# Performance work log

Measured on AMD Instinct MI355X. Metric: run time of the kernel, lower is better.

The kernel has to match this reference:

```python
import jax, jax.numpy as jnp
import numpy as np

GROUPS = 32
EPS = 1e-6  # flax.linen.GroupNorm default


def group_norm(x, scale, bias):
    B, H, W, C = x.shape
    xg = x.reshape(B, H, W, GROUPS, C // GROUPS)
    mean = jnp.mean(xg, axis=(1, 2, 4), keepdims=True)
    var = jnp.var(xg, axis=(1, 2, 4), keepdims=True)
    xn = (xg - mean) * jax.lax.rsqrt(var + EPS)
    return xn.reshape(B, H, W, C) * scale + bias


def setup_inputs() -> dict:
    key = jax.random.key(0)
    ks = jax.random.split(key, 8)
    B, H, W, C = 8, 64, 64, 128
    s = C ** -0.5  # fan-in style init scale for 1x1 conv kernels
    return {
        "x": jax.random.normal(ks[0], (B, H, W, C), dtype=jnp.float32),
        "gn_scale": jnp.ones((C,), dtype=jnp.float32),
        "gn_bias": jnp.zeros((C,), dtype=jnp.float32),
        "wq": jax.random.normal(ks[1], (C, C), dtype=jnp.float32) * s,
        "bq": jnp.zeros((C,), dtype=jnp.float32),
        "wk": jax.random.normal(ks[2], (C, C), dtype=jnp.float32) * s,
        "bk": jnp.zeros((C,), dtype=jnp.float32),
        "wv": jax.random.normal(ks[3], (C, C), dtype=jnp.float32) * s,
        "bv": jnp.zeros((C,), dtype=jnp.float32),
        "wo": jax.random.normal(ks[4], (C, C), dtype=jnp.float32) * s,
        "bo": jnp.zeros((C,), dtype=jnp.float32),
    }


def reference(x, gn_scale, gn_bias, wq, bq, wk, bk, wv, bv, wo, bo):
    B, H, W, C = x.shape
    N = H * W
    h = group_norm(x, gn_scale, gn_bias)                       # [B,H,W,C]
    hf = h.reshape(B, N, C)
    q = hf @ wq + bq                                           # 1x1 conv == per-position matmul
    k = hf @ wk + bk
    v = hf @ wv + bv
    w_ = jnp.einsum('bqd,bkd->bqk', q, k) * (C ** -0.5)        # [B,N,N] full score matrix
    w_ = jax.nn.softmax(w_, axis=2)
    o = jnp.einsum('bqk,bkd->bqd', w_, v)                      # [B,N,C]
    o = o @ wo + bo
    return x + o.reshape(B, H, W, C)
```

## Files before the change

### kernel.cpp

```cpp
#include <hip/hip_runtime.h>
#include <hip/hip_bf16.h>

#define NN 4096
#define CC 128
#define SCALE 0.088388347648318447f
#define LOG2E 1.4426950408889634f

typedef __attribute__((ext_vector_type(8))) short short8v;
typedef __attribute__((ext_vector_type(4))) float f32x4;
typedef __attribute__((ext_vector_type(16))) float f32x16;

#define Z16 {0.f,0.f,0.f,0.f,0.f,0.f,0.f,0.f,0.f,0.f,0.f,0.f,0.f,0.f,0.f,0.f}

__device__ __forceinline__ short f2bf(float f) {
  unsigned u = __float_as_uint(f);
  u = (u + 0x7FFFu + ((u >> 16) & 1u)) >> 16;
  return (short)u;
}
__device__ __forceinline__ float bf2f(short s) {
  return __uint_as_float(((unsigned)(unsigned short)s) << 16);
}
__device__ __forceinline__ unsigned pk2bf(float lo, float hi) {
  unsigned r;
  asm("v_cvt_pk_bf16_f32 %0, %1, %2" : "=v"(r) : "v"(lo), "v"(hi));
  return r;
}
__device__ __forceinline__ f32x4 mfma16(short8v a, short8v b, f32x4 c) {
  return __builtin_amdgcn_mfma_f32_16x16x32_bf16(a, b, c, 0, 0, 0);
}
__device__ __forceinline__ f32x16 mfma32(short8v a, short8v b, f32x16 c) {
  return __builtin_amdgcn_mfma_f32_32x32x16_bf16(a, b, c, 0, 0, 0);
}
__device__ __forceinline__ void gload16(const void* g, void* l) {
  __builtin_amdgcn_global_load_lds(
      (const __attribute__((address_space(1))) unsigned*)g,
      (__attribute__((address_space(3))) unsigned*)l, 16, 0, 0);
}

__global__ __launch_bounds__(256) void convw_k(
    const float* __restrict__ wq, const float* __restrict__ wk,
    const float* __restrict__ wv, const float* __restrict__ wo,
    const float* __restrict__ bq, short* __restrict__ wT,
    float* __restrict__ bqs) {
  int gid = blockIdx.x * 256 + threadIdx.x;
  int widx = gid >> 14, e = gid & 16383;
  int kk = e >> 7, n = e & 127;
  const float* src = (widx == 0) ? wq : (widx == 1) ? wk : (widx == 2) ? wv : wo;
  float v = src[kk * 128 + n];
  if (widx == 0) v *= SCALE * LOG2E;
  wT[widx * 16384 + n * 128 + kk] = f2bf(v);
  if (gid < 128) bqs[gid] = bq[gid] * SCALE * LOG2E;
}

__global__ __launch_bounds__(256) void gnstat_k(const float* __restrict__ x,
    float* __restrict__ mean, float* __restrict__ rstd) {
  int bg = blockIdx.x;
  const float* xp = x + (size_t)(bg >> 5) * NN * CC + (bg & 31) * 4;
  float s = 0.f, ss = 0.f;
  for (int n = threadIdx.x; n < NN; n += 256) {
    float4 v = *reinterpret_cast<const float4*>(xp + (size_t)n * CC);
    s  += v.x + v.y + v.z + v.w;
    ss += v.x * v.x + v.y * v.y + v.z * v.z + v.w * v.w;
  }
  #pragma unroll
  for (int m = 1; m < 64; m <<= 1) {
    s += __shfl_xor(s, m, 64);
    ss += __shfl_xor(ss, m, 64);
  }
  __shared__ float rs[4], rss[4];
  int wid = threadIdx.x >> 6;
  if ((threadIdx.x & 63) == 0) { rs[wid] = s; rss[wid] = ss; }
  __syncthreads();
  if (threadIdx.x == 0) {
    s = rs[0] + rs[1] + rs[2] + rs[3];
    ss = rss[0] + rss[1] + rss[2] + rss[3];
    float mu = s * (1.f / 16384.f);
    float var = ss * (1.f / 16384.f) - mu * mu;
    mean[bg] = mu;
    rstd[bg] = rsqrtf(var + 1e-6f);
  }
}

__global__ __launch_bounds__(256) void gnapply_k(const float* __restrict__ x,
    const float* __restrict__ mean, const float* __restrict__ rstd,
    const float* __restrict__ gsc, const float* __restrict__ gbi,
    short* __restrict__ h) {
  int idx = blockIdx.x * 256 + threadIdx.x;
  int row = idx >> 5, g = idx & 31;
  int bg = ((row >> 12) << 5) | g;
  float4 v  = *reinterpret_cast<const float4*>(x + (size_t)row * CC + g * 4);
  float4 sc = *reinterpret_cast<const float4*>(gsc + g * 4);
  float4 bi = *reinterpret_cast<const float4*>(gbi + g * 4);
  float mu = mean[bg], r = rstd[bg];
  short4 o;
  o.x = f2bf((v.x - mu) * r * sc.x + bi.x);
  o.y = f2bf((v.y - mu) * r * sc.y + bi.y);
  o.z = f2bf((v.z - mu) * r * sc.z + bi.z);
  o.w = f2bf((v.w - mu) * r * sc.w + bi.w);
  *reinterpret_cast<short4*>(h + (size_t)row * CC + g * 4) = o;
}

template <int TRANS>
__global__ __launch_bounds__(256) void proj_k(const short* __restrict__ h,
    const short* __restrict__ wT, const float* __restrict__ bias,
    short* __restrict__ out) {
  __shared__ short wlds[128][136];
  int lane = threadIdx.x & 63, wid = threadIdx.x >> 6;
  for (int i = threadIdx.x; i < 2048; i += 256) {
    int n = i >> 4, kk = (i & 15) << 3;
    *reinterpret_cast<short8v*>(&wlds[n][kk]) =
        *reinterpret_cast<const short8v*>(wT + n * 128 + kk);
  }
  int row0 = blockIdx.x * 64 + wid * 16;
  int arow = row0 + (lane & 15);
  short8v a[4];
  #pragma unroll
  for (int dt = 0; dt < 4; ++dt)
    a[dt] = *reinterpret_cast<const short8v*>(
        h + (size_t)arow * 128 + dt * 32 + ((lane >> 4) << 3));
  __syncthreads();
  f32x4 zero = {0.f, 0.f, 0.f, 0.f};
  f32x4 acc[8];
  #pragma unroll
  for (int nt = 0; nt < 8; ++nt) acc[nt] = zero;
  #pragma unroll
  for (int nt = 0; nt < 8; ++nt) {
    #pragma unroll
    for (int kk = 0; kk < 4; ++kk) {
      short8v b = *reinterpret_cast<const short8v*>(
          &wlds[nt * 16 + (lane & 15)][kk * 32 + ((lane >> 4) << 3)]);
      acc[nt] = mfma16(a[kk], b, acc[nt]);
    }
  }
  #pragma unroll
  for (int nt = 0; nt < 8; ++nt) {
    #pragma unroll
    for (int r = 0; r < 4; ++r) {
      int row = row0 + ((lane >> 4) << 2) + r;
      int col = nt * 16 + (lane & 15);
      float v = acc[nt][r] + bias[col];
      if (TRANS) {
        int b_ = row >> 12, n = row & 4095;
        out[((size_t)b_ * 128 + col) * 4096 + n] = f2bf(v);
      } else {
        out[(size_t)row * 128 + col] = f2bf(v);
      }
    }
  }
}

__global__ __launch_bounds__(256) void projo_k(const short* __restrict__ o,
    const short* __restrict__ wT, const float* __restrict__ bias,
    const float* __restrict__ x, float* __restrict__ out) {
  __shared__ short wlds[128][136];
  int lane = threadIdx.x & 63, wid = threadIdx.x >> 6;
  for (int i = threadIdx.x; i < 2048; i += 256) {
    int n = i >> 4, kk = (i & 15) << 3;
    *reinterpret_cast<short8v*>(&wlds[n][kk]) =
        *reinterpret_cast<const short8v*>(wT + n * 128 + kk);
  }
  int row0 = blockIdx.x * 64 + wid * 16;
  int arow = row0 + (lane & 15);
  short8v a[4];
  #pragma unroll
  for (int dt = 0; dt < 4; ++dt)
    a[dt] = *reinterpret_cast<const short8v*>(
        o + (size_t)arow * 128 + dt * 32 + ((lane >> 4) << 3));
  __syncthreads();
  f32x4 zero = {0.f, 0.f, 0.f, 0.f};
  f32x4 acc[8];
  #pragma unroll
  for (int nt = 0; nt < 8; ++nt) acc[nt] = zero;
  #pragma unroll
  for (int nt = 0; nt < 8; ++nt) {
    #pragma unroll
    for (int kk = 0; kk < 4; ++kk) {
      short8v b = *reinterpret_cast<const short8v*>(
          &wlds[nt * 16 + (lane & 15)][kk * 32 + ((lane >> 4) << 3)]);
      acc[nt] = mfma16(a[kk], b, acc[nt]);
    }
  }
  #pragma unroll
  for (int nt = 0; nt < 8; ++nt) {
    #pragma unroll
    for (int r = 0; r < 4; ++r) {
      int row = row0 + ((lane >> 4) << 2) + r;
      int col = nt * 16 + (lane & 15);
      out[(size_t)row * 128 + col] =
          acc[nt][r] + bias[col] + x[(size_t)row * 128 + col];
    }
  }
}

template <int S>
__global__ __launch_bounds__(512, 2) void attn2_k(
    const short* __restrict__ q, const short* __restrict__ k,
    const short* __restrict__ vt, short* __restrict__ opart,
    float* __restrict__ ms, float* __restrict__ ls) {
  constexpr int KVLEN = NN / S;
  constexpr int NIT = KVLEN / 64;
  __shared__ short8v smem_v[4096];
  char* smem = (char*)smem_v;
  const int tid = threadIdx.x;
  const int lane = tid & 63, warp = tid >> 6;
  const int hh = lane >> 5, ql = lane & 31;
  const int split = (S == 2) ? ((int)blockIdx.x & 1) : 0;
  const int qb_lin = (S == 2) ? ((int)blockIdx.x >> 1) : (int)blockIdx.x;
  const int b = qb_lin >> 4, qblk = qb_lin & 15;
  const int kv0 = split * KVLEN;

  const size_t bqko = (size_t)b * NN * CC;
  short8v qf[8];
  {
    int qrow = qblk * 256 + warp * 32 + ql;
    const short* qp = q + bqko + (size_t)qrow * CC + hh * 8;
    #pragma unroll
    for (int dc = 0; dc < 8; ++dc)
      qf[dc] = *reinterpret_cast<const short8v*>(qp + dc * 16);
  }
  const char* kg = (const char*)(k + bqko);
  const char* vg = (const char*)(vt + (size_t)b * CC * NN);
  const int kr = tid >> 4;
  const int ksw = 16 * ((tid & 15) ^ (kr & 7));
  const int vd = tid >> 3;
  const int vsw = 16 * ((tid & 7) ^ (vd & 7));

  auto stage = [&](int buf, int it) {
    const int kvo = kv0 + it * 64;
    char* base = smem + buf * 32768;
    #pragma unroll
    for (int c = 0; c < 2; ++c) {
      gload16(kg + (size_t)(kvo + c * 32 + kr) * 256 + ksw,
              base + c * 8192 + warp * 1024);
      gload16(vg + (size_t)(c * 64 + vd) * 8192 + (size_t)kvo * 2 + vsw,
              base + 16384 + c * 8192 + warp * 1024);
    }
  };

  f32x16 oacc[4] = {Z16, Z16, Z16, Z16};
  float m_run = -1e30f, l_run = 0.f;

  stage(0, 0);
  asm volatile("s_waitcnt vmcnt(0)" ::: "memory");
  __builtin_amdgcn_s_barrier();

  const int swz = (ql & 7) << 4;
  for (int it = 0; it < NIT; ++it) {
    const int cur = it & 1;
    if (it + 1 < NIT) stage(cur ^ 1, it + 1);

    const char* kb_ = smem + cur * 32768;
    f32x16 sT[2] = {Z16, Z16};
    #pragma unroll
    for (int kt = 0; kt < 2; ++kt) {
      const char* kr_p = kb_ + (32 * kt + ql) * 256;
      #pragma unroll
      for (int dc = 0; dc < 8; ++dc) {
        short8v kf = *reinterpret_cast<const short8v*>(
            kr_p + ((32 * dc + 16 * hh) ^ swz));
        sT[kt] = mfma32(kf, qf[dc], sT[kt]);
      }
    }

    float pmax = -1e30f;
    #pragma unroll
    for (int kt = 0; kt < 2; ++kt)
      #pragma unroll
      for (int r = 0; r < 16; ++r) pmax = fmaxf(pmax, sT[kt][r]);
    pmax = fmaxf(pmax, __shfl_xor(pmax, 32));
    if (!__all(pmax <= m_run + 8.f)) {
      float mn = fmaxf(m_run, pmax);
      float corr = exp2f(m_run - mn);
      m_run = mn; l_run *= corr;
      #pragma unroll
      for (int r = 0; r < 16; ++r) {
        float cr = __shfl(corr, (r & 3) + 8 * (r >> 2) + 4 * hh);
        #pragma unroll
        for (int dt = 0; dt < 4; ++dt) oacc[dt][r] *= cr;
      }
    }
    float rsum = 0.f;
    #pragma unroll
    for (int kt = 0; kt < 2; ++kt)
      #pragma unroll
      for (int r = 0; r < 16; ++r) {
        float p = exp2f(sT[kt][r] - m_run);
        sT[kt][r] = p; rsum += p;
      }
    rsum += __shfl_xor(rsum, 32);
    l_run += rsum;

    const char* vb_ = smem + cur * 32768 + 16384;
    #pragma unroll
    for (int st = 0; st < 4; ++st) {
      const int kt = st >> 1, rb = 8 * (st & 1);
      unsigned w0, w1, w2, w3;
      {
        unsigned xlo = pk2bf(sT[kt][rb + 0], sT[kt][rb + 1]);
        unsigned xhi = pk2bf(sT[kt][rb + 4], sT[kt][rb + 5]);
        unsigned xlx = (unsigned)__shfl_xor((int)xlo, 32);
        unsigned xhx = (unsigned)__shfl_xor((int)xhi, 32);
        w0 = hh ? xhx : xlo;
        w2 = hh ? xhi : xlx;
      }
      {
        unsigned xlo = pk2bf(sT[kt][rb + 2], sT[kt][rb + 3]);
        unsigned xhi = pk2bf(sT[kt][rb + 6], sT[kt][rb + 7]);
        unsigned xlx = (unsigned)__shfl_xor((int)xlo, 32);
        unsigned xhx = (unsigned)__shfl_xor((int)xhi, 32);
        w1 = hh ? xhx : xlo;
        w3 = hh ? xhi : xlx;
      }
      union { unsigned u[4]; short8v v; } pu;
      pu.u[0] = w0; pu.u[1] = w1; pu.u[2] = w2; pu.u[3] = w3;
      #pragma unroll
      for (int dt = 0; dt < 4; ++dt) {
        const char* vr_p = vb_ + (32 * dt + ql) * 128;
        short8v vf = *reinterpret_cast<const short8v*>(
            vr_p + ((32 * st + 16 * hh) ^ swz));
        oacc[dt] = mfma32(pu.v, vf, oacc[dt]);
      }
    }

    asm volatile("s_waitcnt vmcnt(0)" ::: "memory");
    __builtin_amdgcn_s_barrier();
  }

  float rinv = 1.f / l_run;
  short* op = opart + ((size_t)(split * 8 + b) * NN + qblk * 256 + warp * 32) * CC;
  #pragma unroll
  for (int r = 0; r < 16; ++r) {
    int qp = (r & 3) + 8 * (r >> 2) + 4 * hh;
    float ri = __shfl(rinv, qp);
    #pragma unroll
    for (int dt = 0; dt < 4; ++dt)
      op[(size_t)qp * CC + 32 * dt + ql] = f2bf(oacc[dt][r] * ri);
  }
  if (hh == 0) {
    size_t ix = (size_t)(split * 8 + b) * NN + qblk * 256 + warp * 32 + ql;
    ms[ix] = m_run; ls[ix] = l_run;
  }
}

__global__ __launch_bounds__(256) void comb_k(const short* __restrict__ opart,
    const float* __restrict__ ms, const float* __restrict__ ls,
    short* __restrict__ obuf) {
  int gid = blockIdx.x * 256 + threadIdx.x;
  int row = gid >> 4, cg = (gid & 15) << 3;
  float m0 = ms[row], m1 = ms[row + 32768];
  float l0 = ls[row], l1 = ls[row + 32768];
  float M = fmaxf(m0, m1);
  float a0 = exp2f(m0 - M) * l0, a1 = exp2f(m1 - M) * l1;
  float inv = 1.f / (a0 + a1);
  a0 *= inv; a1 *= inv;
  short8v v0 = *reinterpret_cast<const short8v*>(opart + (size_t)row * CC + cg);
  short8v v1 = *reinterpret_cast<const short8v*>(
      opart + ((size_t)row + 32768) * CC + cg);
  short8v o;
  #pragma unroll
  for (int e = 0; e < 8; ++e)
    o[e] = f2bf(bf2f(v0[e]) * a0 + bf2f(v1[e]) * a1);
  *reinterpret_cast<short8v*>(obuf + (size_t)row * CC + cg) = o;
}

extern "C" void kernel_launch(void* const* d_in, const int* in_sizes, int n_in,
                              void* d_out, int out_size, void* d_ws, size_t ws_size,
                              hipStream_t stream) {
  (void)in_sizes; (void)n_in; (void)out_size;
  const float* x   = (const float*)d_in[0];
  const float* gsc = (const float*)d_in[1];
  const float* gbi = (const float*)d_in[2];
  const float* wq  = (const float*)d_in[3];
  const float* bq  = (const float*)d_in[4];
  const float* wk  = (const float*)d_in[5];
  const float* bk  = (const float*)d_in[6];
  const float* wv  = (const float*)d_in[7];
  const float* bv  = (const float*)d_in[8];
  const float* wo  = (const float*)d_in[9];
  const float* bo  = (const float*)d_in[10];
  float* out = (float*)d_out;

  char* ws = (char*)d_ws;
  constexpr size_t OFF_WT   = 0;
  constexpr size_t OFF_BQS  = 131072;
  constexpr size_t OFF_MEAN = 131584;
  constexpr size_t OFF_RSTD = 132608;
  constexpr size_t OFF_MS   = 133632;
  constexpr size_t OFF_LS   = OFF_MS + 262144;
  constexpr size_t OFF_QB   = 658432;
  constexpr size_t OFF_KB   = OFF_QB + 8388608;
  constexpr size_t OFF_VT   = OFF_KB + 8388608;
  constexpr size_t OFF_X    = OFF_VT + 8388608;
  constexpr size_t NEED2    = OFF_X + 16777216;

  short* wT   = (short*)(ws + OFF_WT);
  float* bqs  = (float*)(ws + OFF_BQS);
  float* mean = (float*)(ws + OFF_MEAN);
  float* rstd = (float*)(ws + OFF_RSTD);
  float* ms   = (float*)(ws + OFF_MS);
  float* ls   = (float*)(ws + OFF_LS);
  short* qb   = (short*)(ws + OFF_QB);
  short* kb   = (short*)(ws + OFF_KB);
  short* vtb  = (short*)(ws + OFF_VT);
  short* h    = (short*)(ws + OFF_X);
  short* opart= (short*)(ws + OFF_X);
  const int S = (ws_size >= NEED2) ? 2 : 1;
  short* obuf = (S == 2) ? qb : opart;

  convw_k<<<256, 256, 0, stream>>>(wq, wk, wv, wo, bq, wT, bqs);
  gnstat_k<<<256, 256, 0, stream>>>(x, mean, rstd);
  gnapply_k<<<4096, 256, 0, stream>>>(x, mean, rstd, gsc, gbi, h);
  proj_k<0><<<512, 256, 0, stream>>>(h, wT,         bqs, qb);
  proj_k<0><<<512, 256, 0, stream>>>(h, wT + 16384, bk,  kb);
  proj_k<1><<<512, 256, 0, stream>>>(h, wT + 32768, bv,  vtb);
  if (S == 2) {
    attn2_k<2><<<256, 512, 0, stream>>>(qb, kb, vtb, opart, ms, ls);
    comb_k<<<2048, 256, 0, stream>>>(opart, ms, ls, obuf);
  } else {
    attn2_k<1><<<128, 512, 0, stream>>>(qb, kb, vtb, opart, ms, ls);
  }
  projo_k<<<512, 256, 0, stream>>>(obuf, wT + 49152, bo, x, out);
}
```

Before: 147.8 us.

## Fuse prep, groupnorm+QKV projections, split-KV combine into output projection; use 4-way split

Merges weight conversion with group-norm statistics into one launch, and fuses group-norm apply with all three QKV projections so the normalized activations never go to memory. The split-KV combine is folded into the output projection kernel. The attention split count rises to 4 when the workspace is large enough, with launch bounds raised to 4 blocks per CU for more occupancy. Risks are register pressure under the tighter launch bound, extra partial-output traffic with four splits, and serialized weight reloads across the three projection phases.

```diff
diff --git a/kernel.cpp b/kernel.cpp
--- a/kernel.cpp
+++ b/kernel.cpp
@@ -37,23 +37,25 @@
       (__attribute__((address_space(3))) unsigned*)l, 16, 0, 0);
 }
 
-__global__ __launch_bounds__(256) void convw_k(
+__global__ __launch_bounds__(256) void prep_k(
+    const float* __restrict__ x,
     const float* __restrict__ wq, const float* __restrict__ wk,
     const float* __restrict__ wv, const float* __restrict__ wo,
     const float* __restrict__ bq, short* __restrict__ wT,
-    float* __restrict__ bqs) {
-  int gid = blockIdx.x * 256 + threadIdx.x;
-  int widx = gid >> 14, e = gid & 16383;
-  int kk = e >> 7, n = e & 127;
-  const float* src = (widx == 0) ? wq : (widx == 1) ? wk : (widx == 2) ? wv : wo;
-  float v = src[kk * 128 + n];
-  if (widx == 0) v *= SCALE * LOG2E;
-  wT[widx * 16384 + n * 128 + kk] = f2bf(v);
-  if (gid < 128) bqs[gid] = bq[gid] * SCALE * LOG2E;
-}
-
-__global__ __launch_bounds__(256) void gnstat_k(const float* __restrict__ x,
-    float* __restrict__ mean, float* __restrict__ rstd) {
+    float* __restrict__ bqs, float* __restrict__ mean,
+    float* __restrict__ rstd) {
+  if (blockIdx.x >= 256) {
+    int gid = (blockIdx.x - 256) * 256 + threadIdx.x;
+    int widx = gid >> 14, e = gid & 16383;
+    int kk = e >> 7, n = e & 127;
+    const float* src = (widx == 0) ? wq : (widx == 1) ? wk
+                     : (widx == 2) ? wv : wo;
+    float v = src[kk * 128 + n];
+    if (widx == 0) v *= SCALE * LOG2E;
+    wT[widx * 16384 + n * 128 + kk] = f2bf(v);
+    if (gid < 128) bqs[gid] = bq[gid] * SCALE * LOG2E;
+    return;
+  }
   int bg = blockIdx.x;
   const float* xp = x + (size_t)(bg >> 5) * NN * CC + (bg & 31) * 4;
   float s = 0.f, ss = 0.f;
@@ -81,119 +83,87 @@
   }
 }
 
-__global__ __launch_bounds__(256) void gnapply_k(const float* __restrict__ x,
-    const float* __restrict__ mean, const float* __restrict__ rstd,
-    const float* __restrict__ gsc, const float* __restrict__ gbi,
-    short* __restrict__ h) {
-  int idx = blockIdx.x * 256 + threadIdx.x;
-  int row = idx >> 5, g = idx & 31;
-  int bg = ((row >> 12) << 5) | g;
-  float4 v  = *reinterpret_cast<const float4*>(x + (size_t)row * CC + g * 4);
-  float4 sc = *reinterpret_cast<const float4*>(gsc + g * 4);
-  float4 bi = *reinterpret_cast<const float4*>(gbi + g * 4);
-  float mu = mean[bg], r = rstd[bg];
-  short4 o;
-  o.x = f2bf((v.x - mu) * r * sc.x + bi.x);
-  o.y = f2bf((v.y - mu) * r * sc.y + bi.y);
-  o.z = f2bf((v.z - mu) * r * sc.z + bi.z);
-  o.w = f2bf((v.w - mu) * r * sc.w + bi.w);
-  *reinterpret_cast<short4*>(h + (size_t)row * CC + g * 4) = o;
-}
-
-template <int TRANS>
-__global__ __launch_bounds__(256) void proj_k(const short* __restrict__ h,
-    const short* __restrict__ wT, const float* __restrict__ bias,
-    short* __restrict__ out) {
+__global__ __launch_bounds__(256) void fqkv_k(
+    const float* __restrict__ x, const float* __restrict__ mean,
+    const float* __restrict__ rstd, const float* __restrict__ gsc,
+    const float* __restrict__ gbi, const short* __restrict__ wT,
+    const float* __restrict__ bqs, const float* __restrict__ bk,
+    const float* __restrict__ bv, short* __restrict__ qout,
+    short* __restrict__ kout, short* __restrict__ vtout) {
   __shared__ short wlds[128][136];
   int lane = threadIdx.x & 63, wid = threadIdx.x >> 6;
-  for (int i = threadIdx.x; i < 2048; i += 256) {
-    int n = i >> 4, kk = (i & 15) << 3;
-    *reinterpret_cast<short8v*>(&wlds[n][kk]) =
-        *reinterpret_cast<const short8v*>(wT + n * 128 + kk);
-  }
   int row0 = blockIdx.x * 64 + wid * 16;
   int arow = row0 + (lane & 15);
+  int q4 = lane >> 4;
+  int bidx = arow >> 12;
   short8v a[4];
   #pragma unroll
-  for (int dt = 0; dt < 4; ++dt)
-    a[dt] = *reinterpret_cast<const short8v*>(
-        h + (size_t)arow * 128 + dt * 32 + ((lane >> 4) << 3));
-  __syncthreads();
-  f32x4 zero = {0.f, 0.f, 0.f, 0.f};
-  f32x4 acc[8];
-  #pragma unroll
-  for (int nt = 0; nt < 8; ++nt) acc[nt] = zero;
-  #pragma unroll
-  for (int nt = 0; nt < 8; ++nt) {
-    #pragma unroll
-    for (int kk = 0; kk < 4; ++kk) {
-      short8v b = *reinterpret_cast<const short8v*>(
-          &wlds[nt * 16 + (lane & 15)][kk * 32 + ((lane >> 4) << 3)]);
-      acc[nt] = mfma16(a[kk], b, acc[nt]);
-    }
-  }
-  #pragma unroll
-  for (int nt = 0; nt < 8; ++nt) {
-    #pragma unroll
-    for (int r = 0; r < 4; ++r) {
-      int row = row0 + ((lane >> 4) << 2) + r;
-      int col = nt * 16 + (lane & 15);
-      float v = acc[nt][r] + bias[col];
-      if (TRANS) {
-        int b_ = row >> 12, n = row & 4095;
-        out[((size_t)b_ * 128 + col) * 4096 + n] = f2bf(v);
-      } else {
-        out[(size_t)row * 128 + col] = f2bf(v);
-      }
-    }
-  }
-}
-
-__global__ __launch_bounds__(256) void projo_k(const short* __restrict__ o,
-    const short* __restrict__ wT, const float* __restrict__ bias,
-    const float* __restrict__ x, float* __restrict__ out) {
-  __shared__ short wlds[128][136];
-  int lane = threadIdx.x & 63, wid = threadIdx.x >> 6;
-  for (int i = threadIdx.x; i < 2048; i += 256) {
-    int n = i >> 4, kk = (i & 15) << 3;
-    *reinterpret_cast<short8v*>(&wlds[n][kk]) =
-        *reinterpret_cast<const short8v*>(wT + n * 128 + kk);
-  }
-  int row0 = blockIdx.x * 64 + wid * 16;
-  int arow = row0 + (lane & 15);
-  short8v a[4];
-  #pragma unroll
-  for (int dt = 0; dt < 4; ++dt)
-    a[dt] = *reinterpret_cast<const short8v*>(
-        o + (size_t)arow * 128 + dt * 32 + ((lane >> 4) << 3));
-  __syncthreads();
-  f32x4 zero = {0.f, 0.f, 0.f, 0.f};
-  f32x4 acc[8];
-  #pragma unroll
-  for (int nt = 0; nt < 8; ++nt) acc[nt] = zero;
-  #pragma unroll
-  for (int nt = 0; nt < 8; ++nt) {
-    #pragma unroll
-    for (int kk = 0; kk < 4; ++kk) {
-      short8v b = *reinterpret_cast<const short8v*>(
-          &wlds[nt * 16 + (lane & 15)][kk * 32 + ((lane >> 4) << 3)]);
-      acc[nt] = mfma16(a[kk], b, acc[nt]);
-    }
-  }
-  #pragma unroll
-  for (int nt = 0; nt < 8; ++nt) {
-    #pragma unroll
-    for (int r = 0; r < 4; ++r) {
-      int row = row0 + ((lane >> 4) << 2) + r;
-      int col = nt * 16 + (lane & 15);
-      out[(size_t)row * 128 + col] =
-          acc[nt][r] + bias[col] + x[(size_t)row * 128 + col];
+  for (int dt = 0; dt < 4; ++dt) {
+    int c0 = dt * 32 + q4 * 8;
+    float4 v0 = *reinterpret_cast<const float4*>(x + (size_t)arow * CC + c0);
+    float4 v1 = *reinterpret_cast<const float4*>(x + (size_t)arow * CC + c0 + 4);
+    int g0 = bidx * 32 + (c0 >> 2);
+    float mu0 = mean[g0], r0 = rstd[g0];
+    float mu1 = mean[g0 + 1], r1 = rstd[g0 + 1];
+    float4 s0 = *reinterpret_cast<const float4*>(gsc + c0);
+    float4 s1 = *reinterpret_cast<const float4*>(gsc + c0 + 4);
+    float4 b0 = *reinterpret_cast<const float4*>(gbi + c0);
+    float4 b1 = *reinterpret_cast<const float4*>(gbi + c0 + 4);
+    union { short s[8]; short8v v; } pk;
+    pk.s[0] = f2bf((v0.x - mu0) * r0 * s0.x + b0.x);
+    pk.s[1] = f2bf((v0.y - mu0) * r0 * s0.y + b0.y);
+    pk.s[2] = f2bf((v0.z - mu0) * r0 * s0.z + b0.z);
+    pk.s[3] = f2bf((v0.w - mu0) * r0 * s0.w + b0.w);
+    pk.s[4] = f2bf((v1.x - mu1) * r1 * s1.x + b1.x);
+    pk.s[5] = f2bf((v1.y - mu1) * r1 * s1.y + b1.y);
+    pk.s[6] = f2bf((v1.z - mu1) * r1 * s1.z + b1.z);
+    pk.s[7] = f2bf((v1.w - mu1) * r1 * s1.w + b1.w);
+    a[dt] = pk.v;
+  }
+  for (int ph = 0; ph < 3; ++ph) {
+    if (ph) __syncthreads();
+    const short* w = wT + ph * 16384;
+    for (int i = threadIdx.x; i < 2048; i += 256) {
+      int n = i >> 4, kk = (i & 15) << 3;
+      *reinterpret_cast<short8v*>(&wlds[n][kk]) =
+          *reinterpret_cast<const short8v*>(w + n * 128 + kk);
+    }
+    __syncthreads();
+    const float* bias = (ph == 0) ? bqs : (ph == 1) ? bk : bv;
+    f32x4 zero = {0.f, 0.f, 0.f, 0.f};
+    f32x4 acc[8];
+    #pragma unroll
+    for (int nt = 0; nt < 8; ++nt) acc[nt] = zero;
+    #pragma unroll
+    for (int nt = 0; nt < 8; ++nt) {
+      #pragma unroll
+      for (int kk = 0; kk < 4; ++kk) {
+        short8v b = *reinterpret_cast<const short8v*>(
+            &wlds[nt * 16 + (lane & 15)][kk * 32 + q4 * 8]);
+        acc[nt] = mfma16(a[kk], b, acc[nt]);
+      }
+    }
+    short* dst = (ph == 0) ? qout : (ph == 1) ? kout : vtout;
+    #pragma unroll
+    for (int nt = 0; nt < 8; ++nt) {
+      #pragma unroll
+      for (int r = 0; r < 4; ++r) {
+        int row = row0 + q4 * 4 + r;
+        int col = nt * 16 + (lane & 15);
+        float v = acc[nt][r] + bias[col];
+        if (ph == 2) {
+          int b_ = row >> 12, n = row & 4095;
+          dst[((size_t)b_ * 128 + col) * 4096 + n] = f2bf(v);
+        } else {
+          dst[(size_t)row * 128 + col] = f2bf(v);
+        }
+      }
     }
   }
 }
 
 template <int S>
-__global__ __launch_bounds__(512, 2) void attn2_k(
+__global__ __launch_bounds__(512, 4) void attn2_k(
     const short* __restrict__ q, const short* __restrict__ k,
     const short* __restrict__ vt, short* __restrict__ opart,
     float* __restrict__ ms, float* __restrict__ ls) {
@@ -204,8 +174,8 @@
   const int tid = threadIdx.x;
   const int lane = tid & 63, warp = tid >> 6;
   const int hh = lane >> 5, ql = lane & 31;
-  const int split = (S == 2) ? ((int)blockIdx.x & 1) : 0;
-  const int qb_lin = (S == 2) ? ((int)blockIdx.x >> 1) : (int)blockIdx.x;
+  const int split = (int)blockIdx.x % S;
+  const int qb_lin = (int)blockIdx.x / S;
   const int b = qb_lin >> 4, qblk = qb_lin & 15;
   const int kv0 = split * KVLEN;
 
@@ -342,25 +312,78 @@
   }
 }
 
-__global__ __launch_bounds__(256) void comb_k(const short* __restrict__ opart,
+template <int S>
+__global__ __launch_bounds__(256) void projoc_k(const short* __restrict__ opart,
     const float* __restrict__ ms, const float* __restrict__ ls,
-    short* __restrict__ obuf) {
-  int gid = blockIdx.x * 256 + threadIdx.x;
-  int row = gid >> 4, cg = (gid & 15) << 3;
-  float m0 = ms[row], m1 = ms[row + 32768];
-  float l0 = ls[row], l1 = ls[row + 32768];
-  float M = fmaxf(m0, m1);
-  float a0 = exp2f(m0 - M) * l0, a1 = exp2f(m1 - M) * l1;
-  float inv = 1.f / (a0 + a1);
-  a0 *= inv; a1 *= inv;
-  short8v v0 = *reinterpret_cast<const short8v*>(opart + (size_t)row * CC + cg);
-  short8v v1 = *reinterpret_cast<const short8v*>(
-      opart + ((size_t)row + 32768) * CC + cg);
-  short8v o;
-  #pragma unroll
-  for (int e = 0; e < 8; ++e)
-    o[e] = f2bf(bf2f(v0[e]) * a0 + bf2f(v1[e]) * a1);
-  *reinterpret_cast<short8v*>(obuf + (size_t)row * CC + cg) = o;
+    const short* __restrict__ wT, const float* __restrict__ bias,
+    const float* __restrict__ x, float* __restrict__ out) {
+  __shared__ short wlds[128][136];
+  int lane = threadIdx.x & 63, wid = threadIdx.x >> 6;
+  for (int i = threadIdx.x; i < 2048; i += 256) {
+    int n = i >> 4, kk = (i & 15) << 3;
+    *reinterpret_cast<short8v*>(&wlds[n][kk]) =
+        *reinterpret_cast<const short8v*>(wT + n * 128 + kk);
+  }
+  int row0 = blockIdx.x * 64 + wid * 16;
+  int arow = row0 + (lane & 15);
+  int q4 = lane >> 4;
+  float wgt[S];
+  {
+    float m[S], l[S], M = -1e30f;
+    #pragma unroll
+    for (int s = 0; s < S; ++s) {
+      m[s] = ms[(size_t)s * 32768 + arow];
+      l[s] = ls[(size_t)s * 32768 + arow];
+      M = fmaxf(M, m[s]);
+    }
+    float tot = 0.f;
+    #pragma unroll
+    for (int s = 0; s < S; ++s) { wgt[s] = exp2f(m[s] - M) * l[s]; tot += wgt[s]; }
+    float inv = 1.f / tot;
+    #pragma unroll
+    for (int s = 0; s < S; ++s) wgt[s] *= inv;
+  }
+  short8v a[4];
+  #pragma unroll
+  for (int dt = 0; dt < 4; ++dt) {
+    int c0 = dt * 32 + q4 * 8;
+    float acc8[8] = {0.f, 0.f, 0.f, 0.f, 0.f, 0.f, 0.f, 0.f};
+    #pragma unroll
+    for (int s = 0; s < S; ++s) {
+      short8v v = *reinterpret_cast<const short8v*>(
+          opart + ((size_t)s * 32768 + arow) * CC + c0);
+      #pragma unroll
+      for (int e = 0; e < 8; ++e) acc8[e] += wgt[s] * bf2f(v[e]);
+    }
+    union { short s[8]; short8v v; } pk;
+    #pragma unroll
+    for (int e = 0; e < 8; ++e) pk.s[e] = f2bf(acc8[e]);
+    a[dt] = pk.v;
+  }
+  __syncthreads();
+  f32x4 zero = {0.f, 0.f, 0.f, 0.f};
+  f32x4 acc[8];
+  #pragma unroll
+  for (int nt = 0; nt < 8; ++nt) acc[nt] = zero;
+  #pragma unroll
+  for (int nt = 0; nt < 8; ++nt) {
+    #pragma unroll
+    for (int kk = 0; kk < 4; ++kk) {
+      short8v b = *reinterpret_cast<const short8v*>(
+          &wlds[nt * 16 + (lane & 15)][kk * 32 + q4 * 8]);
+      acc[nt] = mfma16(a[kk], b, acc[nt]);
+    }
+  }
+  #pragma unroll
+  for (int nt = 0; nt < 8; ++nt) {
+    #pragma unroll
+    for (int r = 0; r < 4; ++r) {
+      int row = row0 + q4 * 4 + r;
+      int col = nt * 16 + (lane & 15);
+      out[(size_t)row * 128 + col] =
+          acc[nt][r] + bias[col] + x[(size_t)row * 128 + col];
+    }
+  }
 }
 
 extern "C" void kernel_launch(void* const* d_in, const int* in_sizes, int n_in,
@@ -385,39 +408,36 @@
   constexpr size_t OFF_BQS  = 131072;
   constexpr size_t OFF_MEAN = 131584;
   constexpr size_t OFF_RSTD = 132608;
-  constexpr size_t OFF_MS   = 133632;
-  constexpr size_t OFF_LS   = OFF_MS + 262144;
-  constexpr size_t OFF_QB   = 658432;
+  constexpr size_t OFF_QB   = 133632;
   constexpr size_t OFF_KB   = OFF_QB + 8388608;
   constexpr size_t OFF_VT   = OFF_KB + 8388608;
-  constexpr size_t OFF_X    = OFF_VT + 8388608;
-  constexpr size_t NEED2    = OFF_X + 16777216;
+  constexpr size_t OFF_OP   = OFF_VT + 8388608;
+  constexpr size_t NEED4 = OFF_OP + 4 * 8388608 + 2 * 4 * 131072;
+  constexpr size_t NEED2 = OFF_OP + 2 * 8388608 + 2 * 2 * 131072;
 
   short* wT   = (short*)(ws + OFF_WT);
   float* bqs  = (float*)(ws + OFF_BQS);
   float* mean = (float*)(ws + OFF_MEAN);
   float* rstd = (float*)(ws + OFF_RSTD);
-  float* ms   = (float*)(ws + OFF_MS);
-  float* ls   = (float*)(ws + OFF_LS);
   short* qb   = (short*)(ws + OFF_QB);
   short* kb   = (short*)(ws + OFF_KB);
   short* vtb  = (short*)(ws + OFF_VT);
-  short* h    = (short*)(ws + OFF_X);
-  short* opart= (short*)(ws + OFF_X);
-  const int S = (ws_size >= NEED2) ? 2 : 1;
-  short* obuf = (S == 2) ? qb : opart;
-
-  convw_k<<<256, 256, 0, stream>>>(wq, wk, wv, wo, bq, wT, bqs);
-  gnstat_k<<<256, 256, 0, stream>>>(x, mean, rstd);
-  gnapply_k<<<4096, 256, 0, stream>>>(x, mean, rstd, gsc, gbi, h);
-  proj_k<0><<<512, 256, 0, stream>>>(h, wT,         bqs, qb);
-  proj_k<0><<<512, 256, 0, stream>>>(h, wT + 16384, bk,  kb);
-  proj_k<1><<<512, 256, 0, stream>>>(h, wT + 32768, bv,  vtb);
-  if (S == 2) {
+  short* opart= (short*)(ws + OFF_OP);
+  const int S = (ws_size >= NEED4) ? 4 : (ws_size >= NEED2) ? 2 : 1;
+  float* ms = (float*)(ws + OFF_OP + (size_t)S * 8388608);
+  float* ls = (float*)(ws + OFF_OP + (size_t)S * 8388608 + (size_t)S * 131072);
+
+  prep_k<<<512, 256, 0, stream>>>(x, wq, wk, wv, wo, bq, wT, bqs, mean, rstd);
+  fqkv_k<<<512, 256, 0, stream>>>(x, mean, rstd, gsc, gbi, wT, bqs, bk, bv,
+                                  qb, kb, vtb);
+  if (S == 4) {
+    attn2_k<4><<<512, 512, 0, stream>>>(qb, kb, vtb, opart, ms, ls);
+    projoc_k<4><<<512, 256, 0, stream>>>(opart, ms, ls, wT + 49152, bo, x, out);
+  } else if (S == 2) {
     attn2_k<2><<<256, 512, 0, stream>>>(qb, kb, vtb, opart, ms, ls);
-    comb_k<<<2048, 256, 0, stream>>>(opart, ms, ls, obuf);
+    projoc_k<2><<<512, 256, 0, stream>>>(opart, ms, ls, wT + 49152, bo, x, out);
   } else {
     attn2_k<1><<<128, 512, 0, stream>>>(qb, kb, vtb, opart, ms, ls);
-  }
-  projo_k<<<512, 256, 0, stream>>>(obuf, wT + 49152, bo, x, out);
-}
+    projoc_k<1><<<512, 256, 0, stream>>>(opart, ms, ls, wT + 49152, bo, x, out);
+  }
+}
```

Measured after the change: 280.8 us. 89.9% more time.
